# Kernel optimization log

Hardware: AMD Instinct MI355X
Metric: run time of the kernel (lower is better)

Reference implementation:

```python
import jax, jax.numpy as jnp
from jax import lax
import numpy as np

T = 140
H = 64
B = 8192

def _uniform(key, shape, k):
    return jax.random.uniform(key, shape, dtype=jnp.float32, minval=-k, maxval=k)

def setup_inputs() -> dict:
    key = jax.random.key(0)
    ks = jax.random.split(key, 12)
    k = 1.0 / np.sqrt(H)  # torch default init bound
    return {
        "x": jax.random.normal(ks[0], (B, T, 1), dtype=jnp.float32),
        "h_state": jnp.zeros((2, B, H), dtype=jnp.float32),
        "W_ih0": _uniform(ks[1], (H, 1), k),
        "W_hh0": _uniform(ks[2], (H, H), k),
        "b_ih0": _uniform(ks[3], (H,), k),
        "b_hh0": _uniform(ks[4], (H,), k),
        "W_ih1": _uniform(ks[5], (H, H), k),
        "W_hh1": _uniform(ks[6], (H, H), k),
        "b_ih1": _uniform(ks[7], (H,), k),
        "b_hh1": _uniform(ks[8], (H,), k),
        "W_out": _uniform(ks[9], (1, H), k),
        "b_out": _uniform(ks[10], (1,), k),
    }

def reference(x, h_state, W_ih0, W_hh0, b_ih0, b_hh0, W_ih1, W_hh1, b_ih1, b_hh1, W_out, b_out):
    b = x.shape[0]
    x = x.reshape(b, T, 1)
    xs = jnp.swapaxes(x, 0, 1)  # [T, B, 1]

    def step(carry, xt):
        h0, h1 = carry
        # torch RNN cell: h_t = tanh(x W_ih^T + b_ih + h_{t-1} W_hh^T + b_hh)
        h0n = jnp.tanh(xt @ W_ih0.T + b_ih0 + h0 @ W_hh0.T + b_hh0)
        h1n = jnp.tanh(h0n @ W_ih1.T + b_ih1 + h1 @ W_hh1.T + b_hh1)
        return (h0n, h1n), h1n

    (hf0, hf1), ys = lax.scan(step, (h_state[0], h_state[1]), xs)
    ys = jnp.swapaxes(ys, 0, 1)  # [B, T, H]
    out = (ys @ W_out.T + b_out).reshape(b, T, 1)
    h_final = jnp.stack([hf0, hf1])  # [2, B, H]
    return out, h_final
```

## Files before the change

kernel.cpp:

```cpp
#include <hip/hip_runtime.h>

#define TT 140
#define BB 8192
#define HH 64
#define BT 16
#define HS 72
#define FP ((TT - 1) & 1)

typedef _Float16 half8 __attribute__((ext_vector_type(8)));
typedef _Float16 half4 __attribute__((ext_vector_type(4)));
typedef float    f32x4 __attribute__((ext_vector_type(4)));

#define MFMA16(a,b,c) __builtin_amdgcn_mfma_f32_16x16x32_f16(a, b, c, 0, 0, 0)

__device__ __forceinline__ float fast_tanh(float a) {
    float e = __builtin_amdgcn_exp2f(a * 2.88539008178f);
    return 1.0f - 2.0f * __builtin_amdgcn_rcpf(e + 1.0f);
}

__device__ __forceinline__ half8 ld_frag(const _Float16* p) {
    return *(const half8*)__builtin_assume_aligned(p, 16);
}

__device__ __forceinline__ half8 cvt_frag16(const float* p) {
    f32x4 wa = *(const f32x4*)p;
    f32x4 wb = *(const f32x4*)(p + 4);
    half8 h;
    #pragma unroll
    for (int j = 0; j < 8; ++j) h[j] = (_Float16)((j < 4) ? wa[j] : wb[j - 4]);
    return h;
}

__global__ __launch_bounds__(256, 2)
void rnn_kernel(const float* __restrict__ x,
                const float* __restrict__ h_state,
                const float* __restrict__ W_ih0,
                const float* __restrict__ W_hh0,
                const float* __restrict__ b_ih0,
                const float* __restrict__ b_hh0,
                const float* __restrict__ W_ih1,
                const float* __restrict__ W_hh1,
                const float* __restrict__ b_ih1,
                const float* __restrict__ b_hh1,
                const float* __restrict__ W_out,
                const float* __restrict__ b_out,
                float* __restrict__ out)
{
    __shared__ __align__(16) _Float16 h0f[2][BT * HS];
    __shared__ __align__(16) _Float16 h1f[2][BT * HS];
    __shared__ float xs[TT * 17];
    __shared__ float pps[TT * 68];

    const int tid  = threadIdx.x;
    const int w    = tid >> 6;
    const int lane = tid & 63;
    const int col  = lane & 15;
    const int q    = lane >> 4;
    const int b0   = blockIdx.x * BT;

    half8 A0[2], AI[2], AH[2];
    #pragma unroll
    for (int kt = 0; kt < 2; ++kt) {
        const int off = (16 * w + col) * HH + 32 * kt + 8 * q;
        A0[kt] = cvt_frag16(W_hh0 + off);
        AI[kt] = cvt_frag16(W_ih1 + off);
        AH[kt] = cvt_frag16(W_hh1 + off);
    }
    float e00[4], e10[4], e01[4], e11[4];
    #pragma unroll
    for (int r = 0; r < 4; ++r) {
        int j = 16 * w + 4 * q + r;
        e00[r] = b_ih0[j] + b_hh0[j];  e10[r] = W_ih0[j];
        e01[r] = b_ih1[j] + b_hh1[j];  e11[r] = W_out[j];
    }
    const float bout = b_out[0];

    for (int c = 0; c < (TT * BT + 255) / 256; ++c) {
        int i = c * 256 + tid;
        if (i < TT * BT) {
            int t = i >> 4, b = i & 15;
            xs[t * 17 + b] = x[(size_t)(b0 + b) * TT + t];
        }
    }
    #pragma unroll
    for (int c = 0; c < (BT * HH) / 256; ++c) {
        int i = c * 256 + tid;
        int b = i >> 6, u = i & 63;
        h0f[1][b * HS + u] = (_Float16)h_state[(size_t)(b0 + b) * HH + u];
        h1f[1][b * HS + u] = (_Float16)h_state[(size_t)BB * HH + (size_t)(b0 + b) * HH + u];
    }
    __syncthreads();

    for (int p = 0; p <= TT; ++p) {
        const int rb = (p + 1) & 1;
        const int wb = p & 1;
        half8 H0a = ld_frag(&h0f[rb][col * HS + 8 * q]);
        half8 H0b = ld_frag(&h0f[rb][col * HS + 32 + 8 * q]);
        half8 H1a = ld_frag(&h1f[wb][col * HS + 8 * q]);
        half8 H1b = ld_frag(&h1f[wb][col * HS + 32 + 8 * q]);
        float xt  = xs[p * 17 + col];

        if (p < TT) {
            f32x4 c = {0.f, 0.f, 0.f, 0.f};
            c = MFMA16(A0[0], H0a, c);
            c = MFMA16(A0[1], H0b, c);
            half4 h4;
            #pragma unroll
            for (int r = 0; r < 4; ++r) {
                float pre = c[r] + e00[r] + e10[r] * xt;
                h4[r] = (_Float16)fast_tanh(pre);
            }
            *(half4*)(&h0f[wb][col * HS + 16 * w + 4 * q]) = h4;
        }
        if (p >= 1) {
            f32x4 ci = {0.f, 0.f, 0.f, 0.f}, ch = {0.f, 0.f, 0.f, 0.f};
            ci = MFMA16(AI[0], H0a, ci);
            ci = MFMA16(AI[1], H0b, ci);
            ch = MFMA16(AH[0], H1a, ch);
            ch = MFMA16(AH[1], H1b, ch);
            f32x4 a = ci + ch;
            float pr = 0.f;
            half4 h4;
            #pragma unroll
            for (int r = 0; r < 4; ++r) {
                float pre = a[r] + e01[r];
                float hn  = fast_tanh(pre);
                pr += hn * e11[r];
                h4[r] = (_Float16)hn;
            }
            *(half4*)(&h1f[rb][col * HS + 16 * w + 4 * q]) = h4;
            pr += __shfl_xor(pr, 16, 64);
            pr += __shfl_xor(pr, 32, 64);
            if (lane < 16) pps[(p - 1) * 68 + w * 17 + lane] = pr;
        }
        __syncthreads();
    }

    #pragma unroll
    for (int bq = 0; bq < 4; ++bq) {
        int b = 4 * bq + w;
        #pragma unroll
        for (int c = 0; c < 3; ++c) {
            int t = c * 64 + lane;
            if (t < TT)
                out[(size_t)(b0 + b) * TT + t] =
                    pps[t * 68 + b] + pps[t * 68 + 17 + b]
                  + pps[t * 68 + 34 + b] + pps[t * 68 + 51 + b] + bout;
        }
    }
    const size_t OFF = (size_t)BB * TT;
    #pragma unroll
    for (int c = 0; c < (BT * HH) / 256; ++c) {
        int i = c * 256 + tid;
        int b = i >> 6, u = i & 63;
        out[OFF + (size_t)(b0 + b) * HH + u] = (float)h0f[FP][b * HS + u];
        out[OFF + (size_t)BB * HH + (size_t)(b0 + b) * HH + u] = (float)h1f[FP][b * HS + u];
    }
}

extern "C" void kernel_launch(void* const* d_in, const int* in_sizes, int n_in,
                              void* d_out, int out_size, void* d_ws, size_t ws_size,
                              hipStream_t stream) {
    const float* x      = (const float*)d_in[0];
    const float* hst    = (const float*)d_in[1];
    const float* W_ih0  = (const float*)d_in[2];
    const float* W_hh0  = (const float*)d_in[3];
    const float* b_ih0  = (const float*)d_in[4];
    const float* b_hh0  = (const float*)d_in[5];
    const float* W_ih1  = (const float*)d_in[6];
    const float* W_hh1  = (const float*)d_in[7];
    const float* b_ih1  = (const float*)d_in[8];
    const float* b_hh1  = (const float*)d_in[9];
    const float* W_out  = (const float*)d_in[10];
    const float* b_outp = (const float*)d_in[11];
    float* out = (float*)d_out;

    dim3 grid(BB / BT);
    dim3 block(256);
    rnn_kernel<<<grid, block, 0, stream>>>(x, hst, W_ih0, W_hh0, b_ih0, b_hh0,
                                           W_ih1, W_hh1, b_ih1, b_hh1,
                                           W_out, b_outp, out);
}
```

Baseline: 151.1 us.

## Split the two RNN layers across separate wave groups in a 512-thread block

The block doubles from 256 to 512 threads. Waves 0-3 now compute only layer 0 and waves 4-7 only layer 1, running in a skewed pipeline within each step. Each wave holds only its own layer's weight fragments and bias terms, and loads only the hidden-state fragments that layer needs. This shortens each wave's serial per-step chain of MFMA, tanh and LDS traffic, and raises the number of waves that can hide latency. The cost is a larger block synchronising at every step. The launch bound of (512, 4) also caps registers per thread more tightly, which could cause spills.

```diff
diff --git a/kernel.cpp b/kernel.cpp
--- a/kernel.cpp
+++ b/kernel.cpp
@@ -31,7 +31,7 @@
     return h;
 }
 
-__global__ __launch_bounds__(256, 2)
+__global__ __launch_bounds__(512, 4)
 void rnn_kernel(const float* __restrict__ x,
                 const float* __restrict__ h_state,
                 const float* __restrict__ W_ih0,
@@ -53,6 +53,8 @@
 
     const int tid  = threadIdx.x;
     const int w    = tid >> 6;
+    const int grp  = w >> 2;
+    const int wl   = w & 3;
     const int lane = tid & 63;
     const int col  = lane & 15;
     const int q    = lane >> 4;
@@ -61,30 +63,35 @@
     half8 A0[2], AI[2], AH[2];
     #pragma unroll
     for (int kt = 0; kt < 2; ++kt) {
-        const int off = (16 * w + col) * HH + 32 * kt + 8 * q;
-        A0[kt] = cvt_frag16(W_hh0 + off);
-        AI[kt] = cvt_frag16(W_ih1 + off);
-        AH[kt] = cvt_frag16(W_hh1 + off);
+        const int off = (16 * wl + col) * HH + 32 * kt + 8 * q;
+        if (grp == 0) {
+            A0[kt] = cvt_frag16(W_hh0 + off);
+            AI[kt] = A0[kt]; AH[kt] = A0[kt];
+        } else {
+            AI[kt] = cvt_frag16(W_ih1 + off);
+            AH[kt] = cvt_frag16(W_hh1 + off);
+            A0[kt] = AI[kt];
+        }
     }
-    float e00[4], e10[4], e01[4], e11[4];
+    float e0[4], e1[4];
     #pragma unroll
     for (int r = 0; r < 4; ++r) {
-        int j = 16 * w + 4 * q + r;
-        e00[r] = b_ih0[j] + b_hh0[j];  e10[r] = W_ih0[j];
-        e01[r] = b_ih1[j] + b_hh1[j];  e11[r] = W_out[j];
+        int j = 16 * wl + 4 * q + r;
+        if (grp == 0) { e0[r] = b_ih0[j] + b_hh0[j]; e1[r] = W_ih0[j]; }
+        else          { e0[r] = b_ih1[j] + b_hh1[j]; e1[r] = W_out[j]; }
     }
     const float bout = b_out[0];
 
-    for (int c = 0; c < (TT * BT + 255) / 256; ++c) {
-        int i = c * 256 + tid;
+    for (int c = 0; c < (TT * BT + 511) / 512; ++c) {
+        int i = c * 512 + tid;
         if (i < TT * BT) {
             int t = i >> 4, b = i & 15;
             xs[t * 17 + b] = x[(size_t)(b0 + b) * TT + t];
         }
     }
     #pragma unroll
-    for (int c = 0; c < (BT * HH) / 256; ++c) {
-        int i = c * 256 + tid;
+    for (int c = 0; c < (BT * HH) / 512; ++c) {
+        int i = c * 512 + tid;
         int b = i >> 6, u = i & 63;
         h0f[1][b * HS + u] = (_Float16)h_state[(size_t)(b0 + b) * HH + u];
         h1f[1][b * HS + u] = (_Float16)h_state[(size_t)BB * HH + (size_t)(b0 + b) * HH + u];
@@ -92,53 +99,58 @@
     __syncthreads();
 
     for (int p = 0; p <= TT; ++p) {
-        const int rb = (p + 1) & 1;
-        const int wb = p & 1;
-        half8 H0a = ld_frag(&h0f[rb][col * HS + 8 * q]);
-        half8 H0b = ld_frag(&h0f[rb][col * HS + 32 + 8 * q]);
-        half8 H1a = ld_frag(&h1f[wb][col * HS + 8 * q]);
-        half8 H1b = ld_frag(&h1f[wb][col * HS + 32 + 8 * q]);
-        float xt  = xs[p * 17 + col];
-
-        if (p < TT) {
-            f32x4 c = {0.f, 0.f, 0.f, 0.f};
-            c = MFMA16(A0[0], H0a, c);
-            c = MFMA16(A0[1], H0b, c);
-            half4 h4;
-            #pragma unroll
-            for (int r = 0; r < 4; ++r) {
-                float pre = c[r] + e00[r] + e10[r] * xt;
-                h4[r] = (_Float16)fast_tanh(pre);
+        if (grp == 0) {
+            if (p < TT) {
+                const int rb = (p + 1) & 1, wb = p & 1;
+                half8 H0a = ld_frag(&h0f[rb][col * HS + 8 * q]);
+                half8 H0b = ld_frag(&h0f[rb][col * HS + 32 + 8 * q]);
+                float xt  = xs[p * 17 + col];
+                f32x4 c = {0.f, 0.f, 0.f, 0.f};
+                c = MFMA16(A0[0], H0a, c);
+                c = MFMA16(A0[1], H0b, c);
+                half4 h4;
+                #pragma unroll
+                for (int r = 0; r < 4; ++r) {
+                    float pre = c[r] + e0[r] + e1[r] * xt;
+                    h4[r] = (_Float16)fast_tanh(pre);
+                }
+                *(half4*)(&h0f[wb][col * HS + 16 * wl + 4 * q]) = h4;
             }
-            *(half4*)(&h0f[wb][col * HS + 16 * w + 4 * q]) = h4;
-        }
-        if (p >= 1) {
-            f32x4 ci = {0.f, 0.f, 0.f, 0.f}, ch = {0.f, 0.f, 0.f, 0.f};
-            ci = MFMA16(AI[0], H0a, ci);
-            ci = MFMA16(AI[1], H0b, ci);
-            ch = MFMA16(AH[0], H1a, ch);
-            ch = MFMA16(AH[1], H1b, ch);
-            f32x4 a = ci + ch;
-            float pr = 0.f;
-            half4 h4;
-            #pragma unroll
-            for (int r = 0; r < 4; ++r) {
-                float pre = a[r] + e01[r];
-                float hn  = fast_tanh(pre);
-                pr += hn * e11[r];
-                h4[r] = (_Float16)hn;
+        } else {
+            if (p >= 1) {
+                const int s   = p - 1;
+                const int rb0 = s & 1, rb1 = (s + 1) & 1, wb1 = s & 1;
+                half8 H1a = ld_frag(&h1f[rb1][col * HS + 8 * q]);
+                half8 H1b = ld_frag(&h1f[rb1][col * HS + 32 + 8 * q]);
+                half8 H0a = ld_frag(&h0f[rb0][col * HS + 8 * q]);
+                half8 H0b = ld_frag(&h0f[rb0][col * HS + 32 + 8 * q]);
+                f32x4 ci = {0.f, 0.f, 0.f, 0.f}, ch = {0.f, 0.f, 0.f, 0.f};
+                ch = MFMA16(AH[0], H1a, ch);
+                ch = MFMA16(AH[1], H1b, ch);
+                ci = MFMA16(AI[0], H0a, ci);
+                ci = MFMA16(AI[1], H0b, ci);
+                f32x4 a = ci + ch;
+                float pr = 0.f;
+                half4 h4;
+                #pragma unroll
+                for (int r = 0; r < 4; ++r) {
+                    float pre = a[r] + e0[r];
+                    float hn  = fast_tanh(pre);
+                    pr += hn * e1[r];
+                    h4[r] = (_Float16)hn;
+                }
+                *(half4*)(&h1f[wb1][col * HS + 16 * wl + 4 * q]) = h4;
+                pr += __shfl_xor(pr, 16, 64);
+                pr += __shfl_xor(pr, 32, 64);
+                if (lane < 16) pps[s * 68 + wl * 17 + lane] = pr;
             }
-            *(half4*)(&h1f[rb][col * HS + 16 * w + 4 * q]) = h4;
-            pr += __shfl_xor(pr, 16, 64);
-            pr += __shfl_xor(pr, 32, 64);
-            if (lane < 16) pps[(p - 1) * 68 + w * 17 + lane] = pr;
         }
         __syncthreads();
     }
 
     #pragma unroll
-    for (int bq = 0; bq < 4; ++bq) {
-        int b = 4 * bq + w;
+    for (int bq = 0; bq < 2; ++bq) {
+        int b = 8 * bq + w;
         #pragma unroll
         for (int c = 0; c < 3; ++c) {
             int t = c * 64 + lane;
@@ -150,8 +162,8 @@
     }
     const size_t OFF = (size_t)BB * TT;
     #pragma unroll
-    for (int c = 0; c < (BT * HH) / 256; ++c) {
-        int i = c * 256 + tid;
+    for (int c = 0; c < (BT * HH) / 512; ++c) {
+        int i = c * 512 + tid;
         int b = i >> 6, u = i & 63;
         out[OFF + (size_t)(b0 + b) * HH + u] = (float)h0f[FP][b * HS + u];
         out[OFF + (size_t)BB * HH + (size_t)(b0 + b) * HH + u] = (float)h1f[FP][b * HS + u];
@@ -176,7 +188,7 @@
     float* out = (float*)d_out;
 
     dim3 grid(BB / BT);
-    dim3 block(256);
+    dim3 block(512);
     rnn_kernel<<<grid, block, 0, stream>>>(x, hst, W_ih0, W_hh0, b_ih0, b_hh0,
                                            W_ih1, W_hh1, b_ih1, b_hh1,
                                            W_out, b_outp, out);
```

New measurement: 156.2 us. 1.03x slower.

## Process two 16-row batch tiles per block and compute output projection from h1 fragments

Applied to the files above, without the earlier changes.

Each block now handles 32 batch rows as two 16-row tiles. This reuses the register-held weight fragments across twice the work per barrier and halves the grid to 256 blocks at one block per CU. The output projection moves out of the per-step tanh loop and the pps LDS staging buffer. It is computed one step later from the h1 fragments just read, with one wave per step rotating, and written straight to global memory. This removes the final reduction pass and the large shared buffer, at the cost of an extra loop iteration and lower occupancy.

```diff
diff --git a/kernel.cpp b/kernel.cpp
--- a/kernel.cpp
+++ b/kernel.cpp
@@ -3,7 +3,7 @@
 #define TT 140
 #define BB 8192
 #define HH 64
-#define BT 16
+#define BTW 32
 #define HS 72
 #define FP ((TT - 1) & 1)
 
@@ -31,7 +31,7 @@
     return h;
 }
 
-__global__ __launch_bounds__(256, 2)
+__global__ __launch_bounds__(256, 1)
 void rnn_kernel(const float* __restrict__ x,
                 const float* __restrict__ h_state,
                 const float* __restrict__ W_ih0,
@@ -46,115 +46,132 @@
                 const float* __restrict__ b_out,
                 float* __restrict__ out)
 {
-    __shared__ __align__(16) _Float16 h0f[2][BT * HS];
-    __shared__ __align__(16) _Float16 h1f[2][BT * HS];
-    __shared__ float xs[TT * 17];
-    __shared__ float pps[TT * 68];
+    __shared__ __align__(16) _Float16 h0f[2][2][16 * HS];
+    __shared__ __align__(16) _Float16 h1f[2][2][16 * HS];
+    __shared__ float xs[TT * 33];
 
     const int tid  = threadIdx.x;
-    const int w    = tid >> 6;
+    const int wl   = tid >> 6;
     const int lane = tid & 63;
     const int col  = lane & 15;
     const int q    = lane >> 4;
-    const int b0   = blockIdx.x * BT;
+    const int b0   = blockIdx.x * BTW;
 
     half8 A0[2], AI[2], AH[2];
     #pragma unroll
     for (int kt = 0; kt < 2; ++kt) {
-        const int off = (16 * w + col) * HH + 32 * kt + 8 * q;
+        const int off = (16 * wl + col) * HH + 32 * kt + 8 * q;
         A0[kt] = cvt_frag16(W_hh0 + off);
         AI[kt] = cvt_frag16(W_ih1 + off);
         AH[kt] = cvt_frag16(W_hh1 + off);
     }
-    float e00[4], e10[4], e01[4], e11[4];
+    float e00[4], e10[4], e01[4];
     #pragma unroll
     for (int r = 0; r < 4; ++r) {
-        int j = 16 * w + 4 * q + r;
+        int j = 16 * wl + 4 * q + r;
         e00[r] = b_ih0[j] + b_hh0[j];  e10[r] = W_ih0[j];
-        e01[r] = b_ih1[j] + b_hh1[j];  e11[r] = W_out[j];
+        e01[r] = b_ih1[j] + b_hh1[j];
+    }
+    float WO[16];
+    #pragma unroll
+    for (int j = 0; j < 8; ++j) {
+        WO[j]     = W_out[8 * q + j];
+        WO[8 + j] = W_out[32 + 8 * q + j];
     }
     const float bout = b_out[0];
 
-    for (int c = 0; c < (TT * BT + 255) / 256; ++c) {
+    for (int c = 0; c < (TT * BTW + 255) / 256; ++c) {
         int i = c * 256 + tid;
-        if (i < TT * BT) {
-            int t = i >> 4, b = i & 15;
-            xs[t * 17 + b] = x[(size_t)(b0 + b) * TT + t];
-        }
-    }
-    #pragma unroll
-    for (int c = 0; c < (BT * HH) / 256; ++c) {
+        if (i < TT * BTW) {
+            int t = i >> 5, b = i & 31;
+            xs[t * 33 + b] = x[(size_t)(b0 + b) * TT + t];
+        }
+    }
+    #pragma unroll
+    for (int c = 0; c < (BTW * HH) / 256; ++c) {
         int i = c * 256 + tid;
         int b = i >> 6, u = i & 63;
-        h0f[1][b * HS + u] = (_Float16)h_state[(size_t)(b0 + b) * HH + u];
-        h1f[1][b * HS + u] = (_Float16)h_state[(size_t)BB * HH + (size_t)(b0 + b) * HH + u];
+        int tl = b >> 4, cc = b & 15;
+        h0f[1][tl][cc * HS + u] = (_Float16)h_state[(size_t)(b0 + b) * HH + u];
+        h1f[1][tl][cc * HS + u] = (_Float16)h_state[(size_t)BB * HH + (size_t)(b0 + b) * HH + u];
     }
     __syncthreads();
 
-    for (int p = 0; p <= TT; ++p) {
+    for (int p = 0; p <= TT + 1; ++p) {
         const int rb = (p + 1) & 1;
         const int wb = p & 1;
-        half8 H0a = ld_frag(&h0f[rb][col * HS + 8 * q]);
-        half8 H0b = ld_frag(&h0f[rb][col * HS + 32 + 8 * q]);
-        half8 H1a = ld_frag(&h1f[wb][col * HS + 8 * q]);
-        half8 H1b = ld_frag(&h1f[wb][col * HS + 32 + 8 * q]);
-        float xt  = xs[p * 17 + col];
-
+        half8 H0a[2], H0b[2], H1a[2], H1b[2];
+        float xt[2];
+        #pragma unroll
+        for (int tl = 0; tl < 2; ++tl) {
+            H1a[tl] = ld_frag(&h1f[wb][tl][col * HS + 8 * q]);
+            H1b[tl] = ld_frag(&h1f[wb][tl][col * HS + 32 + 8 * q]);
+        }
+        if (p <= TT) {
+            #pragma unroll
+            for (int tl = 0; tl < 2; ++tl) {
+                H0a[tl] = ld_frag(&h0f[rb][tl][col * HS + 8 * q]);
+                H0b[tl] = ld_frag(&h0f[rb][tl][col * HS + 32 + 8 * q]);
+                xt[tl]  = xs[p * 33 + 16 * tl + col];
+            }
+        }
         if (p < TT) {
-            f32x4 c = {0.f, 0.f, 0.f, 0.f};
-            c = MFMA16(A0[0], H0a, c);
-            c = MFMA16(A0[1], H0b, c);
-            half4 h4;
-            #pragma unroll
-            for (int r = 0; r < 4; ++r) {
-                float pre = c[r] + e00[r] + e10[r] * xt;
-                h4[r] = (_Float16)fast_tanh(pre);
-            }
-            *(half4*)(&h0f[wb][col * HS + 16 * w + 4 * q]) = h4;
-        }
-        if (p >= 1) {
-            f32x4 ci = {0.f, 0.f, 0.f, 0.f}, ch = {0.f, 0.f, 0.f, 0.f};
-            ci = MFMA16(AI[0], H0a, ci);
-            ci = MFMA16(AI[1], H0b, ci);
-            ch = MFMA16(AH[0], H1a, ch);
-            ch = MFMA16(AH[1], H1b, ch);
-            f32x4 a = ci + ch;
-            float pr = 0.f;
-            half4 h4;
-            #pragma unroll
-            for (int r = 0; r < 4; ++r) {
-                float pre = a[r] + e01[r];
-                float hn  = fast_tanh(pre);
-                pr += hn * e11[r];
-                h4[r] = (_Float16)hn;
-            }
-            *(half4*)(&h1f[rb][col * HS + 16 * w + 4 * q]) = h4;
-            pr += __shfl_xor(pr, 16, 64);
-            pr += __shfl_xor(pr, 32, 64);
-            if (lane < 16) pps[(p - 1) * 68 + w * 17 + lane] = pr;
+            #pragma unroll
+            for (int tl = 0; tl < 2; ++tl) {
+                f32x4 c = {0.f, 0.f, 0.f, 0.f};
+                c = MFMA16(A0[0], H0a[tl], c);
+                c = MFMA16(A0[1], H0b[tl], c);
+                half4 h4;
+                #pragma unroll
+                for (int r = 0; r < 4; ++r) {
+                    float pre = c[r] + e00[r] + e10[r] * xt[tl];
+                    h4[r] = (_Float16)fast_tanh(pre);
+                }
+                *(half4*)(&h0f[wb][tl][col * HS + 16 * wl + 4 * q]) = h4;
+            }
+        }
+        if (p >= 1 && p <= TT) {
+            #pragma unroll
+            for (int tl = 0; tl < 2; ++tl) {
+                f32x4 ci = {0.f, 0.f, 0.f, 0.f}, ch = {0.f, 0.f, 0.f, 0.f};
+                ci = MFMA16(AI[0], H0a[tl], ci);
+                ci = MFMA16(AI[1], H0b[tl], ci);
+                ch = MFMA16(AH[0], H1a[tl], ch);
+                ch = MFMA16(AH[1], H1b[tl], ch);
+                f32x4 a = ci + ch;
+                half4 h4;
+                #pragma unroll
+                for (int r = 0; r < 4; ++r)
+                    h4[r] = (_Float16)fast_tanh(a[r] + e01[r]);
+                *(half4*)(&h1f[rb][tl][col * HS + 16 * wl + 4 * q]) = h4;
+            }
+        }
+        if (p >= 2 && wl == ((p - 2) & 3)) {
+            #pragma unroll
+            for (int tl = 0; tl < 2; ++tl) {
+                float pr = 0.f;
+                #pragma unroll
+                for (int j = 0; j < 8; ++j) {
+                    pr += WO[j]     * (float)H1a[tl][j];
+                    pr += WO[8 + j] * (float)H1b[tl][j];
+                }
+                pr += __shfl_xor(pr, 16, 64);
+                pr += __shfl_xor(pr, 32, 64);
+                if (lane < 16)
+                    out[(size_t)(b0 + 16 * tl + lane) * TT + (p - 2)] = pr + bout;
+            }
         }
         __syncthreads();
     }
 
-    #pragma unroll
-    for (int bq = 0; bq < 4; ++bq) {
-        int b = 4 * bq + w;
-        #pragma unroll
-        for (int c = 0; c < 3; ++c) {
-            int t = c * 64 + lane;
-            if (t < TT)
-                out[(size_t)(b0 + b) * TT + t] =
-                    pps[t * 68 + b] + pps[t * 68 + 17 + b]
-                  + pps[t * 68 + 34 + b] + pps[t * 68 + 51 + b] + bout;
-        }
-    }
     const size_t OFF = (size_t)BB * TT;
     #pragma unroll
-    for (int c = 0; c < (BT * HH) / 256; ++c) {
+    for (int c = 0; c < (BTW * HH) / 256; ++c) {
         int i = c * 256 + tid;
         int b = i >> 6, u = i & 63;
-        out[OFF + (size_t)(b0 + b) * HH + u] = (float)h0f[FP][b * HS + u];
-        out[OFF + (size_t)BB * HH + (size_t)(b0 + b) * HH + u] = (float)h1f[FP][b * HS + u];
+        int tl = b >> 4, cc = b & 15;
+        out[OFF + (size_t)(b0 + b) * HH + u] = (float)h0f[FP][tl][cc * HS + u];
+        out[OFF + (size_t)BB * HH + (size_t)(b0 + b) * HH + u] = (float)h1f[FP][tl][cc * HS + u];
     }
 }
 
@@ -175,7 +192,7 @@
     const float* b_outp = (const float*)d_in[11];
     float* out = (float*)d_out;
 
-    dim3 grid(BB / BT);
+    dim3 grid(BB / BTW);
     dim3 block(256);
     rnn_kernel<<<grid, block, 0, stream>>>(x, hst, W_ih0, W_hh0, b_ih0, b_hh0,
                                            W_ih1, W_hh1, b_ih1, b_hh1,
```

Result: slower. 204.9 us (+35.6%).

## Use one wavefront per batch tile to drop block barriers

Applied to the files above, without the earlier changes.

Each block now runs a single 64-lane wavefront that computes all four 16-unit hidden groups itself, instead of four waves each doing one group. This removes the per-step __syncthreads, the double-buffered LDS hidden state and the LDS staging buffer for outputs, which are now written straight to global memory each step. The tanh scale factor is also folded into the fp16 weights and biases. In exchange each wave runs four times as many serial MFMA and tanh steps per timestep. With only 512 single-wave blocks, most SIMDs on the GPU may sit idle, and the per-step output stores are strided rather than coalesced.

```diff
diff --git a/kernel.cpp b/kernel.cpp
--- a/kernel.cpp
+++ b/kernel.cpp
@@ -5,7 +5,7 @@
 #define HH 64
 #define BT 16
 #define HS 72
-#define FP ((TT - 1) & 1)
+#define K_TANH 2.88539008178f
 
 typedef _Float16 half8 __attribute__((ext_vector_type(8)));
 typedef _Float16 half4 __attribute__((ext_vector_type(4)));
@@ -13,8 +13,8 @@
 
 #define MFMA16(a,b,c) __builtin_amdgcn_mfma_f32_16x16x32_f16(a, b, c, 0, 0, 0)
 
-__device__ __forceinline__ float fast_tanh(float a) {
-    float e = __builtin_amdgcn_exp2f(a * 2.88539008178f);
+__device__ __forceinline__ float tanh_ps(float as) {
+    float e = __builtin_amdgcn_exp2f(as);
     return 1.0f - 2.0f * __builtin_amdgcn_rcpf(e + 1.0f);
 }
 
@@ -22,16 +22,17 @@
     return *(const half8*)__builtin_assume_aligned(p, 16);
 }
 
-__device__ __forceinline__ half8 cvt_frag16(const float* p) {
+__device__ __forceinline__ half8 cvt_frag16s(const float* p, float s) {
     f32x4 wa = *(const f32x4*)p;
     f32x4 wb = *(const f32x4*)(p + 4);
     half8 h;
     #pragma unroll
-    for (int j = 0; j < 8; ++j) h[j] = (_Float16)((j < 4) ? wa[j] : wb[j - 4]);
+    for (int j = 0; j < 8; ++j)
+        h[j] = (_Float16)(s * ((j < 4) ? wa[j] : wb[j - 4]));
     return h;
 }
 
-__global__ __launch_bounds__(256, 2)
+__global__ __launch_bounds__(64, 1)
 void rnn_kernel(const float* __restrict__ x,
                 const float* __restrict__ h_state,
                 const float* __restrict__ W_ih0,
@@ -46,115 +47,100 @@
                 const float* __restrict__ b_out,
                 float* __restrict__ out)
 {
-    __shared__ __align__(16) _Float16 h0f[2][BT * HS];
-    __shared__ __align__(16) _Float16 h1f[2][BT * HS];
+    __shared__ __align__(16) _Float16 h0s[BT * HS];
+    __shared__ __align__(16) _Float16 h1s[BT * HS];
     __shared__ float xs[TT * 17];
-    __shared__ float pps[TT * 68];
 
-    const int tid  = threadIdx.x;
-    const int w    = tid >> 6;
-    const int lane = tid & 63;
+    const int lane = threadIdx.x;
     const int col  = lane & 15;
     const int q    = lane >> 4;
     const int b0   = blockIdx.x * BT;
 
-    half8 A0[2], AI[2], AH[2];
+    half8 A0[4][2], AI[4][2], AH[4][2];
+    #pragma unroll
+    for (int g = 0; g < 4; ++g)
     #pragma unroll
     for (int kt = 0; kt < 2; ++kt) {
-        const int off = (16 * w + col) * HH + 32 * kt + 8 * q;
-        A0[kt] = cvt_frag16(W_hh0 + off);
-        AI[kt] = cvt_frag16(W_ih1 + off);
-        AH[kt] = cvt_frag16(W_hh1 + off);
+        const int off = (16 * g + col) * HH + 32 * kt + 8 * q;
+        A0[g][kt] = cvt_frag16s(W_hh0 + off, K_TANH);
+        AI[g][kt] = cvt_frag16s(W_ih1 + off, K_TANH);
+        AH[g][kt] = cvt_frag16s(W_hh1 + off, K_TANH);
     }
-    float e00[4], e10[4], e01[4], e11[4];
+    float e00[4][4], e10[4][4], e01[4][4], WO[4][4];
+    #pragma unroll
+    for (int g = 0; g < 4; ++g)
     #pragma unroll
     for (int r = 0; r < 4; ++r) {
-        int j = 16 * w + 4 * q + r;
-        e00[r] = b_ih0[j] + b_hh0[j];  e10[r] = W_ih0[j];
-        e01[r] = b_ih1[j] + b_hh1[j];  e11[r] = W_out[j];
+        int j = 16 * g + 4 * q + r;
+        e00[g][r] = K_TANH * (b_ih0[j] + b_hh0[j]);
+        e10[g][r] = K_TANH * W_ih0[j];
+        e01[g][r] = K_TANH * (b_ih1[j] + b_hh1[j]);
+        WO[g][r]  = W_out[j];
     }
     const float bout = b_out[0];
 
-    for (int c = 0; c < (TT * BT + 255) / 256; ++c) {
-        int i = c * 256 + tid;
-        if (i < TT * BT) {
-            int t = i >> 4, b = i & 15;
-            xs[t * 17 + b] = x[(size_t)(b0 + b) * TT + t];
-        }
+    for (int i = lane; i < TT * BT; i += 64) {
+        int t = i >> 4, b = i & 15;
+        xs[t * 17 + b] = x[(size_t)(b0 + b) * TT + t];
     }
-    #pragma unroll
-    for (int c = 0; c < (BT * HH) / 256; ++c) {
-        int i = c * 256 + tid;
+    for (int i = lane; i < BT * HH; i += 64) {
         int b = i >> 6, u = i & 63;
-        h0f[1][b * HS + u] = (_Float16)h_state[(size_t)(b0 + b) * HH + u];
-        h1f[1][b * HS + u] = (_Float16)h_state[(size_t)BB * HH + (size_t)(b0 + b) * HH + u];
+        h0s[b * HS + u] = (_Float16)h_state[(size_t)(b0 + b) * HH + u];
+        h1s[b * HS + u] = (_Float16)h_state[(size_t)BB * HH + (size_t)(b0 + b) * HH + u];
     }
     __syncthreads();
 
     for (int p = 0; p <= TT; ++p) {
-        const int rb = (p + 1) & 1;
-        const int wb = p & 1;
-        half8 H0a = ld_frag(&h0f[rb][col * HS + 8 * q]);
-        half8 H0b = ld_frag(&h0f[rb][col * HS + 32 + 8 * q]);
-        half8 H1a = ld_frag(&h1f[wb][col * HS + 8 * q]);
-        half8 H1b = ld_frag(&h1f[wb][col * HS + 32 + 8 * q]);
-        float xt  = xs[p * 17 + col];
+        half8 H0a = ld_frag(&h0s[col * HS + 8 * q]);
+        half8 H0b = ld_frag(&h0s[col * HS + 32 + 8 * q]);
+        half8 H1a = ld_frag(&h1s[col * HS + 8 * q]);
+        half8 H1b = ld_frag(&h1s[col * HS + 32 + 8 * q]);
 
         if (p < TT) {
-            f32x4 c = {0.f, 0.f, 0.f, 0.f};
-            c = MFMA16(A0[0], H0a, c);
-            c = MFMA16(A0[1], H0b, c);
-            half4 h4;
+            float xt = xs[p * 17 + col];
             #pragma unroll
-            for (int r = 0; r < 4; ++r) {
-                float pre = c[r] + e00[r] + e10[r] * xt;
-                h4[r] = (_Float16)fast_tanh(pre);
+            for (int g = 0; g < 4; ++g) {
+                f32x4 c = {0.f, 0.f, 0.f, 0.f};
+                c = MFMA16(A0[g][0], H0a, c);
+                c = MFMA16(A0[g][1], H0b, c);
+                half4 h4;
+                #pragma unroll
+                for (int r = 0; r < 4; ++r)
+                    h4[r] = (_Float16)tanh_ps(c[r] + e00[g][r] + e10[g][r] * xt);
+                *(half4*)(&h0s[col * HS + 16 * g + 4 * q]) = h4;
             }
-            *(half4*)(&h0f[wb][col * HS + 16 * w + 4 * q]) = h4;
         }
         if (p >= 1) {
-            f32x4 ci = {0.f, 0.f, 0.f, 0.f}, ch = {0.f, 0.f, 0.f, 0.f};
-            ci = MFMA16(AI[0], H0a, ci);
-            ci = MFMA16(AI[1], H0b, ci);
-            ch = MFMA16(AH[0], H1a, ch);
-            ch = MFMA16(AH[1], H1b, ch);
-            f32x4 a = ci + ch;
             float pr = 0.f;
-            half4 h4;
             #pragma unroll
-            for (int r = 0; r < 4; ++r) {
-                float pre = a[r] + e01[r];
-                float hn  = fast_tanh(pre);
-                pr += hn * e11[r];
-                h4[r] = (_Float16)hn;
+            for (int g = 0; g < 4; ++g) {
+                f32x4 ci = {0.f, 0.f, 0.f, 0.f}, ch = {0.f, 0.f, 0.f, 0.f};
+                ci = MFMA16(AI[g][0], H0a, ci);
+                ci = MFMA16(AI[g][1], H0b, ci);
+                ch = MFMA16(AH[g][0], H1a, ch);
+                ch = MFMA16(AH[g][1], H1b, ch);
+                f32x4 a = ci + ch;
+                half4 h4;
+                #pragma unroll
+                for (int r = 0; r < 4; ++r) {
+                    float hn = tanh_ps(a[r] + e01[g][r]);
+                    pr += hn * WO[g][r];
+                    h4[r] = (_Float16)hn;
+                }
+                *(half4*)(&h1s[col * HS + 16 * g + 4 * q]) = h4;
             }
-            *(half4*)(&h1f[rb][col * HS + 16 * w + 4 * q]) = h4;
             pr += __shfl_xor(pr, 16, 64);
             pr += __shfl_xor(pr, 32, 64);
-            if (lane < 16) pps[(p - 1) * 68 + w * 17 + lane] = pr;
+            if (lane < 16)
+                out[(size_t)(b0 + lane) * TT + (p - 1)] = pr + bout;
         }
-        __syncthreads();
     }
 
-    #pragma unroll
-    for (int bq = 0; bq < 4; ++bq) {
-        int b = 4 * bq + w;
-        #pragma unroll
-        for (int c = 0; c < 3; ++c) {
-            int t = c * 64 + lane;
-            if (t < TT)
-                out[(size_t)(b0 + b) * TT + t] =
-                    pps[t * 68 + b] + pps[t * 68 + 17 + b]
-                  + pps[t * 68 + 34 + b] + pps[t * 68 + 51 + b] + bout;
-        }
-    }
     const size_t OFF = (size_t)BB * TT;
-    #pragma unroll
-    for (int c = 0; c < (BT * HH) / 256; ++c) {
-        int i = c * 256 + tid;
+    for (int i = lane; i < BT * HH; i += 64) {
         int b = i >> 6, u = i & 63;
-        out[OFF + (size_t)(b0 + b) * HH + u] = (float)h0f[FP][b * HS + u];
-        out[OFF + (size_t)BB * HH + (size_t)(b0 + b) * HH + u] = (float)h1f[FP][b * HS + u];
+        out[OFF + (size_t)(b0 + b) * HH + u] = (float)h0s[b * HS + u];
+        out[OFF + (size_t)BB * HH + (size_t)(b0 + b) * HH + u] = (float)h1s[b * HS + u];
     }
 }
 
@@ -176,7 +162,7 @@
     float* out = (float*)d_out;
 
     dim3 grid(BB / BT);
-    dim3 block(256);
+    dim3 block(64);
     rnn_kernel<<<grid, block, 0, stream>>>(x, hst, W_ih0, W_hh0, b_ih0, b_hh0,
                                            W_ih1, W_hh1, b_ih1, b_hh1,
                                            W_out, b_outp, out);
```

After: 212.1 us. +40.4%, slower.
